# Kernel optimization log

Hardware: AMD Instinct MI355X
Metric: run time of the kernel (lower is better)

## Reference

```python
import jax, jax.numpy as jnp
import numpy as np

B, S, H, D = 256, 512, 256, 512  # batch, n_seq, n_hid, n_dim
LN_EPS = 1e-5


def _xavier(key, fan_out, fan_in):
    lim = (6.0 / (fan_in + fan_out)) ** 0.5
    return jax.random.uniform(key, (fan_out, fan_in), jnp.float32, -lim, lim)


def setup_inputs() -> dict:
    key = jax.random.key(0)
    ks = jax.random.split(key, 10)
    x = jax.random.normal(ks[0], (B, S, D), jnp.float32)
    k_w = _xavier(ks[1], H, D)
    q_w = _xavier(ks[2], H, D)
    v_w = _xavier(ks[3], H, D)
    lb = 1.0 / (D ** 0.5)
    k_b = jax.random.uniform(ks[4], (H,), jnp.float32, -lb, lb)
    q_b = jax.random.uniform(ks[5], (H,), jnp.float32, -lb, lb)
    v_b = jax.random.uniform(ks[6], (H,), jnp.float32, -lb, lb)
    attn_bias = jax.random.normal(ks[7], (S, H), jnp.float32)
    ln_g = jnp.ones((H,), jnp.float32)
    ln_b = jnp.zeros((H,), jnp.float32)
    lo = 1.0 / ((S * H) ** 0.5)
    out_w = jax.random.uniform(ks[8], (D, S * H), jnp.float32, -lo, lo)
    out_b = jax.random.uniform(ks[9], (D,), jnp.float32, -lo, lo)
    return {"x": x, "k_w": k_w, "k_b": k_b, "q_w": q_w, "q_b": q_b,
            "v_w": v_w, "v_b": v_b, "attn_bias": attn_bias,
            "ln_g": ln_g, "ln_b": ln_b, "out_w": out_w, "out_b": out_b}


def reference(x, k_w, k_b, q_w, q_b, v_w, v_b, attn_bias, ln_g, ln_b, out_w, out_b):
    # projections: [B,S,D] -> [B,S,H]
    k = jnp.einsum('bsd,hd->bsh', x, k_w) + k_b
    q = jnp.einsum('bsd,hd->bsh', x, q_w) + q_b
    v = jnp.einsum('bsd,hd->bsh', x, v_w) + v_b
    # scores = k^T q, scaled by BATCH size^-0.5 (faithful to v.shape[0]**-0.5)
    scale = x.shape[0] ** (-0.5)
    scores = jnp.einsum('bsh,bsg->bhg', k, q) * scale  # [B,H,H]
    weight = jax.nn.softmax(scores, axis=1)
    out = jnp.einsum('bsh,bhg->bsg', v, weight)  # [B,S,H]
    out = out + attn_bias
    # LayerNorm over last dim
    mu = out.mean(-1, keepdims=True)
    var = out.var(-1, keepdims=True)
    out = (out - mu) * jax.lax.rsqrt(var + LN_EPS) * ln_g + ln_b
    # dropout is identity in eval mode; exact (erf) GELU matches torch default
    out = jax.nn.gelu(out, approximate=False)
    out = out.reshape(out.shape[0], S * H)
    out = out @ out_w.T + out_b  # [B,D]
    return out[:, None, :]  # [B,1,D]
```

## Files before the change

kernel.cpp:

```cpp
#include <hip/hip_runtime.h>
#include <hip/hip_bf16.h>
#include <math.h>

#define B_ 256
#define S_ 512
#define H_ 256
#define D_ 512

typedef __bf16 bf16;
typedef __bf16 bf16x8 __attribute__((ext_vector_type(8)));
typedef float  f32x4  __attribute__((ext_vector_type(4)));
typedef unsigned short u16x8 __attribute__((ext_vector_type(8)));
typedef unsigned short u16x4 __attribute__((ext_vector_type(4)));

#define MFMA(a, b, c) __builtin_amdgcn_mfma_f32_16x16x32_bf16((a), (b), (c), 0, 0, 0)

__device__ __forceinline__ int swz(int row, int kbyte) {
  return (row * 128 + kbyte) ^ ((row & 7) << 4);
}
__device__ __forceinline__ int pswz(int row, int kbyte) {
  return (row * 512 + kbyte) ^ ((row & 7) << 4);
}
__device__ __forceinline__ unsigned short bfbits(float f) {
  bf16 h = (bf16)f;
  union { bf16 b; unsigned short u; } c; c.b = h; return c.u;
}
__device__ __forceinline__ bf16x8 cvt8(const float* __restrict__ p) {
  f32x4 a = *(const f32x4*)p;
  f32x4 b = *(const f32x4*)(p + 4);
  bf16x8 r;
  r[0] = (bf16)a[0]; r[1] = (bf16)a[1]; r[2] = (bf16)a[2]; r[3] = (bf16)a[3];
  r[4] = (bf16)b[0]; r[5] = (bf16)b[1]; r[6] = (bf16)b[2]; r[7] = (bf16)b[3];
  return r;
}
__device__ __forceinline__ void gload16(const unsigned short* g, unsigned char* l) {
  __builtin_amdgcn_global_load_lds(
      (const __attribute__((address_space(1))) unsigned int*)g,
      (__attribute__((address_space(3))) unsigned int*)l, 16, 0, 0);
}

__global__ __launch_bounds__(256) void k_convw(
    const float* __restrict__ kw, const float* __restrict__ qw,
    const float* __restrict__ vw, unsigned short* __restrict__ wc)
{
  const int r = blockIdx.x;
  const float* src = (r < 256) ? kw + (size_t)r * 512
                   : (r < 512) ? qw + (size_t)(r - 256) * 512
                               : vw + (size_t)(r - 512) * 512;
  const int c = threadIdx.x * 2;
  wc[(size_t)r * 512 + c]     = bfbits(src[c]);
  wc[(size_t)r * 512 + c + 1] = bfbits(src[c + 1]);
}

__global__ __launch_bounds__(256) void k_convx(
    const float* __restrict__ x, unsigned short* __restrict__ xb, int nchunk)
{
  for (int c = blockIdx.x * 256 + threadIdx.x; c < nchunk; c += gridDim.x * 256) {
    bf16x8 v = cvt8(x + (size_t)c * 8);
    *(bf16x8*)(xb + (size_t)c * 8) = v;
  }
}

__global__ __launch_bounds__(256) void k_proj2(
    const unsigned short* __restrict__ xb,
    const unsigned short* __restrict__ wc,
    const float* __restrict__ kbi, const float* __restrict__ qbi,
    const float* __restrict__ vbi,
    unsigned short* __restrict__ k_t, unsigned short* __restrict__ q_t,
    unsigned short* __restrict__ v_o, int cstart, int nwg)
{
  __shared__ __align__(16) unsigned char sA[16384];
  __shared__ __align__(16) unsigned char sB[16384];

  const int o = blockIdx.x;
  const int cpx = nwg >> 3;
  const int a = (o & 7) * cpx + (o >> 3);
  const int mt = a / 6;
  const int nb = a - mt * 6;
  const int m0 = mt * 128;
  const int n0 = nb * 128;
  const int region = nb >> 1;
  const int h0 = (nb & 1) * 128;
  const float* __restrict__ Bi = (region == 0) ? kbi : (region == 1) ? qbi : vbi;

  const int tid = threadIdx.x;
  const int lane = tid & 63;
  const int wid = tid >> 6;
  const int wm = wid >> 1;
  const int wn = wid & 1;

  f32x4 acc[4][4];
#pragma unroll
  for (int i = 0; i < 4; ++i)
#pragma unroll
    for (int j = 0; j < 4; ++j) acc[i][j] = (f32x4){0.f, 0.f, 0.f, 0.f};

  const int lr = lane >> 3;
  const int lk = (lane & 7) << 3;

  for (int kt = 0; kt < 8; ++kt) {
    if (kt) __syncthreads();
#pragma unroll
    for (int i = 0; i < 4; ++i) {
      const int chunk = wid * 4 + i;
      const int row = chunk * 8 + lr;
      gload16(xb + (size_t)(m0 + row) * 512 + kt * 64 + lk, sA + chunk * 1024);
      gload16(wc + (size_t)(n0 + row) * 512 + kt * 64 + lk, sB + chunk * 1024);
    }
    __syncthreads();
#pragma unroll
    for (int ks = 0; ks < 2; ++ks) {
      const int kb2 = ks * 64 + ((lane >> 4) << 4);
      bf16x8 av[4], bv[4];
#pragma unroll
      for (int f = 0; f < 4; ++f)
        av[f] = *(const bf16x8*)(sA + (wm * 64 + f * 16 + (lane & 15)) * 128 + kb2);
#pragma unroll
      for (int f = 0; f < 4; ++f)
        bv[f] = *(const bf16x8*)(sB + (wn * 64 + f * 16 + (lane & 15)) * 128 + kb2);
#pragma unroll
      for (int fm = 0; fm < 4; ++fm)
#pragma unroll
        for (int fn = 0; fn < 4; ++fn)
          acc[fm][fn] = MFMA(av[fm], bv[fn], acc[fm][fn]);
    }
  }

  const int m0g = cstart * 512 + m0;
  const int b = m0g >> 9;
  const int sbase = m0g & 511;
  const int r4 = (lane >> 4) * 4;
#pragma unroll
  for (int fn = 0; fn < 4; ++fn) {
    const int hcol = h0 + wn * 64 + fn * 16 + (lane & 15);
    const float bias = Bi[hcol];
#pragma unroll
    for (int fm = 0; fm < 4; ++fm) {
      const int s = sbase + wm * 64 + fm * 16 + r4;
      if (region < 2) {
        unsigned short* dst = ((region == 0) ? k_t : q_t) +
                              (size_t)b * (H_ * S_) + (size_t)hcol * S_ + s;
        u16x4 ov;
#pragma unroll
        for (int j = 0; j < 4; ++j) ov[j] = bfbits(acc[fm][fn][j] + bias);
        *(u16x4*)dst = ov;
      } else {
#pragma unroll
        for (int j = 0; j < 4; ++j)
          v_o[(size_t)b * (S_ * H_) + (size_t)(s + j) * H_ + hcol] =
              bfbits(acc[fm][fn][j] + bias);
      }
    }
  }
}

__global__ __launch_bounds__(512, 2) void k_attn(
    const unsigned short* __restrict__ k_t,
    const unsigned short* __restrict__ q_t,
    const unsigned short* __restrict__ v_o,
    const float* __restrict__ attn_bias,
    const float* __restrict__ lng, const float* __restrict__ lnb,
    unsigned short* __restrict__ act)
{
  __shared__ __align__(16) unsigned char sP[131072];
  __shared__ float lbuf[2][4][128];

  const int tid = threadIdx.x;
  const int lane = tid & 63;
  const int wid = tid >> 6;
  const int b = blockIdx.x;
  const int l15 = lane & 15;
  const int l16 = lane >> 4;
  const int r4 = l16 * 4;

  const unsigned short* __restrict__ Kb = k_t + (size_t)b * (H_ * S_);
  const unsigned short* __restrict__ Qb = q_t + (size_t)b * (H_ * S_);
  const unsigned short* __restrict__ Vb = v_o + (size_t)b * (S_ * H_);

  unsigned char* sK = sP;
  unsigned char* sQ = sP + 32768;
  float* redm = (float*)(sP + 65536);
  float* reds = (float*)(sP + 67584);

  const int wh = wid >> 2;
  const int wg = wid & 3;

  f32x4 acc1[8][4];
#pragma unroll
  for (int i = 0; i < 8; ++i)
#pragma unroll
    for (int j = 0; j < 4; ++j) acc1[i][j] = (f32x4){0.f, 0.f, 0.f, 0.f};

  for (int kt = 0; kt < 8; ++kt) {
    __syncthreads();
#pragma unroll
    for (int i = 0; i < 4; ++i) {
      int c = tid + i * 512;
      int row = c >> 3, kc = (c & 7) * 8;
      *(u16x8*)(sK + swz(row, kc * 2)) =
          *(const u16x8*)(Kb + (size_t)row * S_ + kt * 64 + kc);
      *(u16x8*)(sQ + swz(row, kc * 2)) =
          *(const u16x8*)(Qb + (size_t)row * S_ + kt * 64 + kc);
    }
    __syncthreads();
#pragma unroll
    for (int ks = 0; ks < 2; ++ks) {
      const int kbyte = ks * 64 + l16 * 16;
      bf16x8 av[8], bv[4];
#pragma unroll
      for (int f = 0; f < 8; ++f)
        av[f] = *(const bf16x8*)(sK + swz(wh * 128 + f * 16 + l15, kbyte));
#pragma unroll
      for (int f = 0; f < 4; ++f)
        bv[f] = *(const bf16x8*)(sQ + swz(wg * 64 + f * 16 + l15, kbyte));
#pragma unroll
      for (int fm = 0; fm < 8; ++fm)
#pragma unroll
        for (int fn = 0; fn < 4; ++fn)
          acc1[fm][fn] = MFMA(av[fm], bv[fn], acc1[fm][fn]);
    }
  }

#pragma unroll
  for (int fm = 0; fm < 8; ++fm)
#pragma unroll
    for (int fn = 0; fn < 4; ++fn)
#pragma unroll
      for (int j = 0; j < 4; ++j) acc1[fm][fn][j] *= 0.0625f;

  float cmax[4] = {-3.0e38f, -3.0e38f, -3.0e38f, -3.0e38f};
#pragma unroll
  for (int fm = 0; fm < 8; ++fm)
#pragma unroll
    for (int fn = 0; fn < 4; ++fn)
#pragma unroll
      for (int j = 0; j < 4; ++j) cmax[fn] = fmaxf(cmax[fn], acc1[fm][fn][j]);
#pragma unroll
  for (int fn = 0; fn < 4; ++fn) {
    cmax[fn] = fmaxf(cmax[fn], __shfl_xor(cmax[fn], 16));
    cmax[fn] = fmaxf(cmax[fn], __shfl_xor(cmax[fn], 32));
  }
  if (lane < 16) {
#pragma unroll
    for (int fn = 0; fn < 4; ++fn)
      redm[wh * 256 + wg * 64 + fn * 16 + lane] = cmax[fn];
  }
  __syncthreads();
  float gmax[4];
#pragma unroll
  for (int fn = 0; fn < 4; ++fn) {
    int c = wg * 64 + fn * 16 + l15;
    gmax[fn] = fmaxf(redm[c], redm[256 + c]);
  }
  float csum[4] = {0.f, 0.f, 0.f, 0.f};
#pragma unroll
  for (int fm = 0; fm < 8; ++fm)
#pragma unroll
    for (int fn = 0; fn < 4; ++fn)
#pragma unroll
      for (int j = 0; j < 4; ++j) {
        float p = __expf(acc1[fm][fn][j] - gmax[fn]);
        acc1[fm][fn][j] = p;
        csum[fn] += p;
      }
#pragma unroll
  for (int fn = 0; fn < 4; ++fn) {
    csum[fn] += __shfl_xor(csum[fn], 16);
    csum[fn] += __shfl_xor(csum[fn], 32);
  }
  if (lane < 16) {
#pragma unroll
    for (int fn = 0; fn < 4; ++fn)
      reds[wh * 256 + wg * 64 + fn * 16 + lane] = csum[fn];
  }
  __syncthreads();
  float ginv[4];
#pragma unroll
  for (int fn = 0; fn < 4; ++fn) {
    int c = wg * 64 + fn * 16 + l15;
    ginv[fn] = 1.0f / (reds[c] + reds[256 + c]);
  }
  __syncthreads();

#pragma unroll
  for (int fn = 0; fn < 4; ++fn) {
    const int g = wg * 64 + fn * 16 + l15;
#pragma unroll
    for (int fm = 0; fm < 8; ++fm) {
      const int h = wh * 128 + fm * 16 + r4;
      u16x4 pv;
#pragma unroll
      for (int j = 0; j < 4; ++j) pv[j] = bfbits(acc1[fm][fn][j] * ginv[fn]);
      *(u16x4*)(sP + pswz(g, h * 2)) = pv;
    }
  }
  __syncthreads();

  const float* __restrict__ bias = attn_bias;
  for (int ms = 0; ms < 4; ++ms) {
    const int s0 = ms * 128 + wh * 64;
    f32x4 acc2[4][4];
#pragma unroll
    for (int i = 0; i < 4; ++i)
#pragma unroll
      for (int j = 0; j < 4; ++j) acc2[i][j] = (f32x4){0.f, 0.f, 0.f, 0.f};

#pragma unroll
    for (int kt = 0; kt < 4; ++kt) {
      bf16x8 av[4][2];
#pragma unroll
      for (int fm = 0; fm < 4; ++fm)
#pragma unroll
        for (int ks = 0; ks < 2; ++ks)
          av[fm][ks] = *(const bf16x8*)(
              Vb + (size_t)(s0 + fm * 16 + l15) * H_ + kt * 64 + ks * 32 + l16 * 8);
#pragma unroll
      for (int ks = 0; ks < 2; ++ks) {
        bf16x8 bv[4];
#pragma unroll
        for (int fn = 0; fn < 4; ++fn)
          bv[fn] = *(const bf16x8*)(
              sP + pswz(wg * 64 + fn * 16 + l15, kt * 128 + ks * 64 + l16 * 16));
#pragma unroll
        for (int fm = 0; fm < 4; ++fm)
#pragma unroll
          for (int fn = 0; fn < 4; ++fn)
            acc2[fm][fn] = MFMA(av[fm][ks], bv[fn], acc2[fm][fn]);
      }
    }

    __syncthreads();
#pragma unroll
    for (int fm = 0; fm < 4; ++fm) {
#pragma unroll
      for (int j = 0; j < 4; ++j) {
        const int rloc = wh * 64 + fm * 16 + r4 + j;
        const int s = ms * 128 + rloc;
        float ps = 0.f, psq = 0.f;
#pragma unroll
        for (int fn = 0; fn < 4; ++fn) {
          int g = wg * 64 + fn * 16 + l15;
          float vv = acc2[fm][fn][j] + bias[(size_t)s * H_ + g];
          acc2[fm][fn][j] = vv;
          ps += vv; psq += vv * vv;
        }
        ps += __shfl_xor(ps, 1);  psq += __shfl_xor(psq, 1);
        ps += __shfl_xor(ps, 2);  psq += __shfl_xor(psq, 2);
        ps += __shfl_xor(ps, 4);  psq += __shfl_xor(psq, 4);
        ps += __shfl_xor(ps, 8);  psq += __shfl_xor(psq, 8);
        if (l15 == 0) { lbuf[0][wg][rloc] = ps; lbuf[1][wg][rloc] = psq; }
      }
    }
    __syncthreads();
#pragma unroll
    for (int fm = 0; fm < 4; ++fm) {
#pragma unroll
      for (int j = 0; j < 4; ++j) {
        const int rloc = wh * 64 + fm * 16 + r4 + j;
        const int s = ms * 128 + rloc;
        float sum = lbuf[0][0][rloc] + lbuf[0][1][rloc] + lbuf[0][2][rloc] + lbuf[0][3][rloc];
        float sq  = lbuf[1][0][rloc] + lbuf[1][1][rloc] + lbuf[1][2][rloc] + lbuf[1][3][rloc];
        float mu = sum * (1.f / H_);
        float var = sq * (1.f / H_) - mu * mu;
        float rstd = rsqrtf(var + 1e-5f);
#pragma unroll
        for (int fn = 0; fn < 4; ++fn) {
          int g = wg * 64 + fn * 16 + l15;
          float xv = (acc2[fm][fn][j] - mu) * rstd * lng[g] + lnb[g];
          float y = 0.5f * xv * (1.f + erff(xv * 0.70710678118654752f));
          act[(size_t)b * (S_ * H_) + (size_t)s * H_ + g] = bfbits(y);
        }
      }
    }
  }
}

__global__ __launch_bounds__(512) void k_final(
    const unsigned short* __restrict__ act,
    const float* __restrict__ ow,
    float* __restrict__ partial)
{
  __shared__ __align__(16) unsigned char sA[256 * 128];
  __shared__ __align__(16) unsigned char sB[64 * 128];

  const int tid = threadIdx.x;
  const int lane = tid & 63;
  const int wid = tid >> 6;
  const int wm = wid >> 1;
  const int wn = wid & 1;
  const int n0 = blockIdx.x * 64;
  const size_t k0 = (size_t)blockIdx.y * 4096;

  f32x4 acc[4][2];
#pragma unroll
  for (int i = 0; i < 4; ++i)
#pragma unroll
    for (int j = 0; j < 2; ++j) acc[i][j] = (f32x4){0.f, 0.f, 0.f, 0.f};

  for (int kt = 0; kt < 64; ++kt) {
    const size_t kb = k0 + kt * 64;
    __syncthreads();
#pragma unroll
    for (int i = 0; i < 4; ++i) {
      int c = tid + i * 512;
      int row = c >> 3, kc = (c & 7) * 8;
      *(u16x8*)(sA + swz(row, kc * 2)) =
          *(const u16x8*)(act + (size_t)row * 131072 + kb + kc);
    }
    {
      int row = tid >> 3, kc = (tid & 7) * 8;
      *(bf16x8*)(sB + swz(row, kc * 2)) =
          cvt8(ow + (size_t)(n0 + row) * 131072 + kb + kc);
    }
    __syncthreads();
#pragma unroll
    for (int ks = 0; ks < 2; ++ks) {
      const int kbyte = ks * 64 + (lane >> 4) * 16;
      bf16x8 av[4], bv[2];
#pragma unroll
      for (int f = 0; f < 4; ++f)
        av[f] = *(const bf16x8*)(sA + swz(wm * 64 + f * 16 + (lane & 15), kbyte));
#pragma unroll
      for (int f = 0; f < 2; ++f)
        bv[f] = *(const bf16x8*)(sB + swz(wn * 32 + f * 16 + (lane & 15), kbyte));
#pragma unroll
      for (int fm = 0; fm < 4; ++fm)
#pragma unroll
        for (int fn = 0; fn < 2; ++fn)
          acc[fm][fn] = MFMA(av[fm], bv[fn], acc[fm][fn]);
    }
  }

  float* __restrict__ P = partial + (size_t)blockIdx.y * (256 * 512);
  const int r4 = (lane >> 4) * 4;
#pragma unroll
  for (int fn = 0; fn < 2; ++fn) {
    int col = n0 + wn * 32 + fn * 16 + (lane & 15);
#pragma unroll
    for (int fm = 0; fm < 4; ++fm) {
      int mb = wm * 64 + fm * 16 + r4;
#pragma unroll
      for (int j = 0; j < 4; ++j)
        P[(size_t)(mb + j) * 512 + col] = acc[fm][fn][j];
    }
  }
}

__global__ __launch_bounds__(256) void k_reduce(
    const float* __restrict__ partial,
    const float* __restrict__ ob,
    float* __restrict__ out)
{
  const int i4 = blockIdx.x * 256 + threadIdx.x;
  f32x4 s = *(const f32x4*)(ob + ((i4 & 127) << 2));
#pragma unroll
  for (int ks = 0; ks < 32; ++ks)
    s += *(const f32x4*)(partial + (size_t)ks * 131072 + (size_t)i4 * 4);
  *(f32x4*)(out + (size_t)i4 * 4) = s;
}

extern "C" void kernel_launch(void* const* d_in, const int* in_sizes, int n_in,
                              void* d_out, int out_size, void* d_ws, size_t ws_size,
                              hipStream_t stream) {
  const float* x         = (const float*)d_in[0];
  const float* k_w       = (const float*)d_in[1];
  const float* k_b       = (const float*)d_in[2];
  const float* q_w       = (const float*)d_in[3];
  const float* q_b       = (const float*)d_in[4];
  const float* v_w       = (const float*)d_in[5];
  const float* v_b       = (const float*)d_in[6];
  const float* attn_bias = (const float*)d_in[7];
  const float* ln_g      = (const float*)d_in[8];
  const float* ln_b      = (const float*)d_in[9];
  const float* out_w     = (const float*)d_in[10];
  const float* out_b     = (const float*)d_in[11];
  float* out = (float*)d_out;

  char* ws = (char*)d_ws;
  unsigned short* k_t = (unsigned short*)(ws);
  unsigned short* q_t = (unsigned short*)(ws + 67108864);
  unsigned short* v_o = (unsigned short*)(ws + 134217728);
  unsigned short* wc  = (unsigned short*)(ws + 201326592);
  unsigned short* xb  = (unsigned short*)(ws + 201326592 + 786432);
  unsigned short* act = k_t;
  float* partial      = (float*)(ws + 67108864);

  k_convw<<<dim3(768), dim3(256), 0, stream>>>(k_w, q_w, v_w, wc);

  const int starts[5] = {0, 56, 112, 168, 224};
  const int nbats[5]  = {56, 56, 56, 56, 32};
  for (int r = 0; r < 5; ++r) {
    const int nbat = nbats[r];
    k_convx<<<dim3(1024), dim3(256), 0, stream>>>(
        x + (size_t)starts[r] * 262144, xb, nbat * 32768);
    const int nwg = nbat * 24;
    k_proj2<<<dim3(nwg), dim3(256), 0, stream>>>(
        xb, wc, k_b, q_b, v_b, k_t, q_t, v_o, starts[r], nwg);
  }

  k_attn<<<dim3(256), dim3(512), 0, stream>>>(
      k_t, q_t, v_o, attn_bias, ln_g, ln_b, act);

  k_final<<<dim3(8, 32), dim3(512), 0, stream>>>(act, out_w, partial);
  k_reduce<<<dim3(128), dim3(256), 0, stream>>>(partial, out_b, out);
}
```

Measured before the change: 517.8 us.

## Fuse x conversion into projection GEMM and widen attention kernel to 1024 threads

The separate fp32-to-bf16 conversion kernel for x and the chunked launch loop are removed. The projection kernel now reads fp32 x directly, converting it while staging into swizzled LDS, and runs as a single 6144-workgroup launch. The attention kernel moves from 512 to 1024 threads per block, splits the score tile across 16 waves, loads K/Q and V through global_load_lds into LDS, and processes the PV product in two halves of 256 rows. This saves an intermediate round trip of x through memory and the extra launches, and raises attention parallelism. In exchange it reads fp32 x once per projection tile instead of bf16, and the attention kernel takes more LDS and synchronisations.

```diff
diff --git a/kernel.cpp b/kernel.cpp
--- a/kernel.cpp
+++ b/kernel.cpp
@@ -17,9 +17,6 @@
 
 __device__ __forceinline__ int swz(int row, int kbyte) {
   return (row * 128 + kbyte) ^ ((row & 7) << 4);
-}
-__device__ __forceinline__ int pswz(int row, int kbyte) {
-  return (row * 512 + kbyte) ^ ((row & 7) << 4);
 }
 __device__ __forceinline__ unsigned short bfbits(float f) {
   bf16 h = (bf16)f;
@@ -52,22 +49,13 @@
   wc[(size_t)r * 512 + c + 1] = bfbits(src[c + 1]);
 }
 
-__global__ __launch_bounds__(256) void k_convx(
-    const float* __restrict__ x, unsigned short* __restrict__ xb, int nchunk)
-{
-  for (int c = blockIdx.x * 256 + threadIdx.x; c < nchunk; c += gridDim.x * 256) {
-    bf16x8 v = cvt8(x + (size_t)c * 8);
-    *(bf16x8*)(xb + (size_t)c * 8) = v;
-  }
-}
-
 __global__ __launch_bounds__(256) void k_proj2(
-    const unsigned short* __restrict__ xb,
+    const float* __restrict__ x,
     const unsigned short* __restrict__ wc,
     const float* __restrict__ kbi, const float* __restrict__ qbi,
     const float* __restrict__ vbi,
     unsigned short* __restrict__ k_t, unsigned short* __restrict__ q_t,
-    unsigned short* __restrict__ v_o, int cstart, int nwg)
+    unsigned short* __restrict__ v_o, int nwg)
 {
   __shared__ __align__(16) unsigned char sA[16384];
   __shared__ __align__(16) unsigned char sB[16384];
@@ -88,6 +76,7 @@
   const int wid = tid >> 6;
   const int wm = wid >> 1;
   const int wn = wid & 1;
+  const int l15 = lane & 15;
 
   f32x4 acc[4][4];
 #pragma unroll
@@ -100,11 +89,17 @@
 
   for (int kt = 0; kt < 8; ++kt) {
     if (kt) __syncthreads();
+#pragma unroll
+    for (int i = 0; i < 4; ++i) {
+      int c = tid + i * 256;
+      int row = c >> 3, kc = (c & 7) * 8;
+      *(bf16x8*)(sA + swz(row, kc * 2)) =
+          cvt8(x + (size_t)(m0 + row) * D_ + kt * 64 + kc);
+    }
 #pragma unroll
     for (int i = 0; i < 4; ++i) {
       const int chunk = wid * 4 + i;
       const int row = chunk * 8 + lr;
-      gload16(xb + (size_t)(m0 + row) * 512 + kt * 64 + lk, sA + chunk * 1024);
       gload16(wc + (size_t)(n0 + row) * 512 + kt * 64 + lk, sB + chunk * 1024);
     }
     __syncthreads();
@@ -114,10 +109,10 @@
       bf16x8 av[4], bv[4];
 #pragma unroll
       for (int f = 0; f < 4; ++f)
-        av[f] = *(const bf16x8*)(sA + (wm * 64 + f * 16 + (lane & 15)) * 128 + kb2);
-#pragma unroll
-      for (int f = 0; f < 4; ++f)
-        bv[f] = *(const bf16x8*)(sB + (wn * 64 + f * 16 + (lane & 15)) * 128 + kb2);
+        av[f] = *(const bf16x8*)(sA + swz(wm * 64 + f * 16 + l15, kb2));
+#pragma unroll
+      for (int f = 0; f < 4; ++f)
+        bv[f] = *(const bf16x8*)(sB + (wn * 64 + f * 16 + l15) * 128 + kb2);
 #pragma unroll
       for (int fm = 0; fm < 4; ++fm)
 #pragma unroll
@@ -126,13 +121,12 @@
     }
   }
 
-  const int m0g = cstart * 512 + m0;
-  const int b = m0g >> 9;
-  const int sbase = m0g & 511;
+  const int b = m0 >> 9;
+  const int sbase = m0 & 511;
   const int r4 = (lane >> 4) * 4;
 #pragma unroll
   for (int fn = 0; fn < 4; ++fn) {
-    const int hcol = h0 + wn * 64 + fn * 16 + (lane & 15);
+    const int hcol = h0 + wn * 64 + fn * 16 + l15;
     const float bias = Bi[hcol];
 #pragma unroll
     for (int fm = 0; fm < 4; ++fm) {
@@ -154,7 +148,7 @@
   }
 }
 
-__global__ __launch_bounds__(512, 2) void k_attn(
+__global__ __launch_bounds__(1024, 4) void k_attn(
     const unsigned short* __restrict__ k_t,
     const unsigned short* __restrict__ q_t,
     const unsigned short* __restrict__ v_o,
@@ -162,79 +156,75 @@
     const float* __restrict__ lng, const float* __restrict__ lnb,
     unsigned short* __restrict__ act)
 {
-  __shared__ __align__(16) unsigned char sP[131072];
-  __shared__ float lbuf[2][4][128];
+  __shared__ __align__(16) unsigned char sm[147456];
+  unsigned char* sP = sm;
+  unsigned char* sK = sm;
+  unsigned char* sQ = sm + 32768;
+  unsigned char* sV = sm + 131072;
+  float* redm = (float*)(sm + 131072);
+  float* reds = (float*)(sm + 131072 + 4096);
+  float* lbuf = (float*)(sm + 131072);
 
   const int tid = threadIdx.x;
   const int lane = tid & 63;
   const int wid = tid >> 6;
-  const int b = blockIdx.x;
   const int l15 = lane & 15;
   const int l16 = lane >> 4;
-  const int r4 = l16 * 4;
+  const int b = blockIdx.x;
+  const int wh = wid >> 2;
+  const int wq = wid & 3;
 
   const unsigned short* __restrict__ Kb = k_t + (size_t)b * (H_ * S_);
   const unsigned short* __restrict__ Qb = q_t + (size_t)b * (H_ * S_);
   const unsigned short* __restrict__ Vb = v_o + (size_t)b * (S_ * H_);
 
-  unsigned char* sK = sP;
-  unsigned char* sQ = sP + 32768;
-  float* redm = (float*)(sP + 65536);
-  float* reds = (float*)(sP + 67584);
-
-  const int wh = wid >> 2;
-  const int wg = wid & 3;
-
-  f32x4 acc1[8][4];
-#pragma unroll
-  for (int i = 0; i < 8; ++i)
+  const int srow8 = lane >> 3;
+  const int scol16 = (lane & 7) ^ srow8;
+
+  f32x4 acc1[4][4];
+#pragma unroll
+  for (int i = 0; i < 4; ++i)
 #pragma unroll
     for (int j = 0; j < 4; ++j) acc1[i][j] = (f32x4){0.f, 0.f, 0.f, 0.f};
 
   for (int kt = 0; kt < 8; ++kt) {
-    __syncthreads();
-#pragma unroll
-    for (int i = 0; i < 4; ++i) {
-      int c = tid + i * 512;
-      int row = c >> 3, kc = (c & 7) * 8;
-      *(u16x8*)(sK + swz(row, kc * 2)) =
-          *(const u16x8*)(Kb + (size_t)row * S_ + kt * 64 + kc);
-      *(u16x8*)(sQ + swz(row, kc * 2)) =
-          *(const u16x8*)(Qb + (size_t)row * S_ + kt * 64 + kc);
+    if (kt) __syncthreads();
+#pragma unroll
+    for (int i = 0; i < 2; ++i) {
+      const int cb = wid * 2 + i;
+      const int row = cb * 8 + srow8;
+      gload16(Kb + (size_t)row * S_ + kt * 64 + scol16 * 8, sK + cb * 1024);
+      gload16(Qb + (size_t)row * S_ + kt * 64 + scol16 * 8, sQ + cb * 1024);
     }
     __syncthreads();
 #pragma unroll
     for (int ks = 0; ks < 2; ++ks) {
-      const int kbyte = ks * 64 + l16 * 16;
-      bf16x8 av[8], bv[4];
-#pragma unroll
-      for (int f = 0; f < 8; ++f)
-        av[f] = *(const bf16x8*)(sK + swz(wh * 128 + f * 16 + l15, kbyte));
-#pragma unroll
-      for (int f = 0; f < 4; ++f)
-        bv[f] = *(const bf16x8*)(sQ + swz(wg * 64 + f * 16 + l15, kbyte));
-#pragma unroll
-      for (int fm = 0; fm < 8; ++fm)
+      const int kb2 = ks * 64 + l16 * 16;
+      bf16x8 av[4], bv[4];
+#pragma unroll
+      for (int f = 0; f < 4; ++f)
+        av[f] = *(const bf16x8*)(sK + swz(wh * 64 + f * 16 + l15, kb2));
+#pragma unroll
+      for (int f = 0; f < 4; ++f)
+        bv[f] = *(const bf16x8*)(sQ + swz(wq * 64 + f * 16 + l15, kb2));
+#pragma unroll
+      for (int fm = 0; fm < 4; ++fm)
 #pragma unroll
         for (int fn = 0; fn < 4; ++fn)
           acc1[fm][fn] = MFMA(av[fm], bv[fn], acc1[fm][fn]);
     }
   }
 
-#pragma unroll
-  for (int fm = 0; fm < 8; ++fm)
+  float cmax[4] = {-3.0e38f, -3.0e38f, -3.0e38f, -3.0e38f};
+#pragma unroll
+  for (int fm = 0; fm < 4; ++fm)
 #pragma unroll
     for (int fn = 0; fn < 4; ++fn)
 #pragma unroll
-      for (int j = 0; j < 4; ++j) acc1[fm][fn][j] *= 0.0625f;
-
-  float cmax[4] = {-3.0e38f, -3.0e38f, -3.0e38f, -3.0e38f};
-#pragma unroll
-  for (int fm = 0; fm < 8; ++fm)
-#pragma unroll
-    for (int fn = 0; fn < 4; ++fn)
-#pragma unroll
-      for (int j = 0; j < 4; ++j) cmax[fn] = fmaxf(cmax[fn], acc1[fm][fn][j]);
+      for (int j = 0; j < 4; ++j) {
+        acc1[fm][fn][j] *= 0.0625f;
+        cmax[fn] = fmaxf(cmax[fn], acc1[fm][fn][j]);
+      }
 #pragma unroll
   for (int fn = 0; fn < 4; ++fn) {
     cmax[fn] = fmaxf(cmax[fn], __shfl_xor(cmax[fn], 16));
@@ -243,18 +233,19 @@
   if (lane < 16) {
 #pragma unroll
     for (int fn = 0; fn < 4; ++fn)
-      redm[wh * 256 + wg * 64 + fn * 16 + lane] = cmax[fn];
+      redm[wh * 256 + wq * 64 + fn * 16 + lane] = cmax[fn];
   }
   __syncthreads();
   float gmax[4];
 #pragma unroll
   for (int fn = 0; fn < 4; ++fn) {
-    int c = wg * 64 + fn * 16 + l15;
-    gmax[fn] = fmaxf(redm[c], redm[256 + c]);
+    const int c = wq * 64 + fn * 16 + l15;
+    gmax[fn] = fmaxf(fmaxf(redm[c], redm[256 + c]),
+                     fmaxf(redm[512 + c], redm[768 + c]));
   }
   float csum[4] = {0.f, 0.f, 0.f, 0.f};
 #pragma unroll
-  for (int fm = 0; fm < 8; ++fm)
+  for (int fm = 0; fm < 4; ++fm)
 #pragma unroll
     for (int fn = 0; fn < 4; ++fn)
 #pragma unroll
@@ -271,102 +262,106 @@
   if (lane < 16) {
 #pragma unroll
     for (int fn = 0; fn < 4; ++fn)
-      reds[wh * 256 + wg * 64 + fn * 16 + lane] = csum[fn];
+      reds[wh * 256 + wq * 64 + fn * 16 + lane] = csum[fn];
   }
   __syncthreads();
-  float ginv[4];
-#pragma unroll
-  for (int fn = 0; fn < 4; ++fn) {
-    int c = wg * 64 + fn * 16 + l15;
-    ginv[fn] = 1.0f / (reds[c] + reds[256 + c]);
-  }
-  __syncthreads();
-
-#pragma unroll
-  for (int fn = 0; fn < 4; ++fn) {
-    const int g = wg * 64 + fn * 16 + l15;
-#pragma unroll
-    for (int fm = 0; fm < 8; ++fm) {
-      const int h = wh * 128 + fm * 16 + r4;
+  float gi[4];
+#pragma unroll
+  for (int fn = 0; fn < 4; ++fn) {
+    const int c = wq * 64 + fn * 16 + l15;
+    gi[fn] = 1.0f / (reds[c] + reds[256 + c] + reds[512 + c] + reds[768 + c]);
+  }
+
+#pragma unroll
+  for (int fn = 0; fn < 4; ++fn) {
+    const int g = wq * 64 + fn * 16 + l15;
+#pragma unroll
+    for (int fm = 0; fm < 4; ++fm) {
+      const int h0 = wh * 64 + fm * 16 + l16 * 4;
       u16x4 pv;
 #pragma unroll
-      for (int j = 0; j < 4; ++j) pv[j] = bfbits(acc1[fm][fn][j] * ginv[fn]);
-      *(u16x4*)(sP + pswz(g, h * 2)) = pv;
-    }
-  }
-  __syncthreads();
-
-  const float* __restrict__ bias = attn_bias;
-  for (int ms = 0; ms < 4; ++ms) {
-    const int s0 = ms * 128 + wh * 64;
+      for (int j = 0; j < 4; ++j) pv[j] = bfbits(acc1[fm][fn][j] * gi[fn]);
+      *(u16x4*)(sP + ((g * 512 + h0 * 2) ^ ((g & 7) << 4))) = pv;
+    }
+  }
+
+  const int vrow = tid >> 2;
+  const int vcol16 = (tid & 3) ^ ((vrow >> 1) & 3);
+
+  for (int so = 0; so < 2; ++so) {
     f32x4 acc2[4][4];
 #pragma unroll
     for (int i = 0; i < 4; ++i)
 #pragma unroll
       for (int j = 0; j < 4; ++j) acc2[i][j] = (f32x4){0.f, 0.f, 0.f, 0.f};
 
-#pragma unroll
-    for (int kt = 0; kt < 4; ++kt) {
-      bf16x8 av[4][2];
-#pragma unroll
-      for (int fm = 0; fm < 4; ++fm)
-#pragma unroll
-        for (int ks = 0; ks < 2; ++ks)
-          av[fm][ks] = *(const bf16x8*)(
-              Vb + (size_t)(s0 + fm * 16 + l15) * H_ + kt * 64 + ks * 32 + l16 * 8);
-#pragma unroll
-      for (int ks = 0; ks < 2; ++ks) {
-        bf16x8 bv[4];
+    for (int kh = 0; kh < 8; ++kh) {
+      __syncthreads();
+      gload16(Vb + (size_t)(so * 256 + vrow) * H_ + kh * 32 + vcol16 * 8,
+              sV + wid * 1024);
+      __syncthreads();
+      bf16x8 av[4], bv[4];
+#pragma unroll
+      for (int f = 0; f < 4; ++f) {
+        const int rl = wh * 64 + f * 16 + l15;
+        av[f] = *(const bf16x8*)(sV + rl * 64 + ((l16 ^ ((rl >> 1) & 3)) << 4));
+      }
+#pragma unroll
+      for (int fn = 0; fn < 4; ++fn) {
+        const int g = wq * 64 + fn * 16 + l15;
+        bv[fn] = *(const bf16x8*)(
+            sP + ((g * 512 + kh * 64 + l16 * 16) ^ ((g & 7) << 4)));
+      }
+#pragma unroll
+      for (int f = 0; f < 4; ++f)
 #pragma unroll
         for (int fn = 0; fn < 4; ++fn)
-          bv[fn] = *(const bf16x8*)(
-              sP + pswz(wg * 64 + fn * 16 + l15, kt * 128 + ks * 64 + l16 * 16));
-#pragma unroll
-        for (int fm = 0; fm < 4; ++fm)
-#pragma unroll
-          for (int fn = 0; fn < 4; ++fn)
-            acc2[fm][fn] = MFMA(av[fm][ks], bv[fn], acc2[fm][fn]);
-      }
-    }
-
-    __syncthreads();
-#pragma unroll
-    for (int fm = 0; fm < 4; ++fm) {
+          acc2[f][fn] = MFMA(av[f], bv[fn], acc2[f][fn]);
+    }
+    __syncthreads();
+
+#pragma unroll
+    for (int f = 0; f < 4; ++f) {
 #pragma unroll
       for (int j = 0; j < 4; ++j) {
-        const int rloc = wh * 64 + fm * 16 + r4 + j;
-        const int s = ms * 128 + rloc;
+        const int rloc = wh * 64 + f * 16 + l16 * 4 + j;
+        const int s = so * 256 + rloc;
         float ps = 0.f, psq = 0.f;
 #pragma unroll
         for (int fn = 0; fn < 4; ++fn) {
-          int g = wg * 64 + fn * 16 + l15;
-          float vv = acc2[fm][fn][j] + bias[(size_t)s * H_ + g];
-          acc2[fm][fn][j] = vv;
+          const int g = wq * 64 + fn * 16 + l15;
+          float vv = acc2[f][fn][j] + attn_bias[(size_t)s * H_ + g];
+          acc2[f][fn][j] = vv;
           ps += vv; psq += vv * vv;
         }
         ps += __shfl_xor(ps, 1);  psq += __shfl_xor(psq, 1);
         ps += __shfl_xor(ps, 2);  psq += __shfl_xor(psq, 2);
         ps += __shfl_xor(ps, 4);  psq += __shfl_xor(psq, 4);
         ps += __shfl_xor(ps, 8);  psq += __shfl_xor(psq, 8);
-        if (l15 == 0) { lbuf[0][wg][rloc] = ps; lbuf[1][wg][rloc] = psq; }
-      }
-    }
-    __syncthreads();
-#pragma unroll
-    for (int fm = 0; fm < 4; ++fm) {
+        if (l15 == 0) {
+          lbuf[wq * 256 + rloc] = ps;
+          lbuf[1024 + wq * 256 + rloc] = psq;
+        }
+      }
+    }
+    __syncthreads();
+#pragma unroll
+    for (int f = 0; f < 4; ++f) {
 #pragma unroll
       for (int j = 0; j < 4; ++j) {
-        const int rloc = wh * 64 + fm * 16 + r4 + j;
-        const int s = ms * 128 + rloc;
-        float sum = lbuf[0][0][rloc] + lbuf[0][1][rloc] + lbuf[0][2][rloc] + lbuf[0][3][rloc];
-        float sq  = lbuf[1][0][rloc] + lbuf[1][1][rloc] + lbuf[1][2][rloc] + lbuf[1][3][rloc];
+        const int rloc = wh * 64 + f * 16 + l16 * 4 + j;
+        const int s = so * 256 + rloc;
+        float sum = lbuf[rloc] + lbuf[256 + rloc] +
+                    lbuf[512 + rloc] + lbuf[768 + rloc];
+        float sq  = lbuf[1024 + rloc] + lbuf[1280 + rloc] +
+                    lbuf[1536 + rloc] + lbuf[1792 + rloc];
         float mu = sum * (1.f / H_);
         float var = sq * (1.f / H_) - mu * mu;
         float rstd = rsqrtf(var + 1e-5f);
 #pragma unroll
         for (int fn = 0; fn < 4; ++fn) {
-          int g = wg * 64 + fn * 16 + l15;
-          float xv = (acc2[fm][fn][j] - mu) * rstd * lng[g] + lnb[g];
+          const int g = wq * 64 + fn * 16 + l15;
+          float xv = (acc2[f][fn][j] - mu) * rstd * lng[g] + lnb[g];
           float y = 0.5f * xv * (1.f + erff(xv * 0.70710678118654752f));
           act[(size_t)b * (S_ * H_) + (size_t)s * H_ + g] = bfbits(y);
         }
@@ -481,24 +476,16 @@
   unsigned short* q_t = (unsigned short*)(ws + 67108864);
   unsigned short* v_o = (unsigned short*)(ws + 134217728);
   unsigned short* wc  = (unsigned short*)(ws + 201326592);
-  unsigned short* xb  = (unsigned short*)(ws + 201326592 + 786432);
   unsigned short* act = k_t;
   float* partial      = (float*)(ws + 67108864);
 
   k_convw<<<dim3(768), dim3(256), 0, stream>>>(k_w, q_w, v_w, wc);
 
-  const int starts[5] = {0, 56, 112, 168, 224};
-  const int nbats[5]  = {56, 56, 56, 56, 32};
-  for (int r = 0; r < 5; ++r) {
-    const int nbat = nbats[r];
-    k_convx<<<dim3(1024), dim3(256), 0, stream>>>(
-        x + (size_t)starts[r] * 262144, xb, nbat * 32768);
-    const int nwg = nbat * 24;
-    k_proj2<<<dim3(nwg), dim3(256), 0, stream>>>(
-        xb, wc, k_b, q_b, v_b, k_t, q_t, v_o, starts[r], nwg);
-  }
-
-  k_attn<<<dim3(256), dim3(512), 0, stream>>>(
+  const int nwg = 6144;
+  k_proj2<<<dim3(nwg), dim3(256), 0, stream>>>(
+      x, wc, k_b, q_b, v_b, k_t, q_t, v_o, nwg);
+
+  k_attn<<<dim3(256), dim3(1024), 0, stream>>>(
       k_t, q_t, v_o, attn_bias, ln_g, ln_b, act);
 
   k_final<<<dim3(8, 32), dim3(512), 0, stream>>>(act, out_w, partial);
```

Result: faster. 476.1 us (-8.1%).
